# Kernel tuning notes

Measured on AMD Instinct MI355X. Metric: run time of the kernel, lower is better.

The kernel has to match this reference:

```python
import jax, jax.numpy as jnp
import numpy as np

B = 8192
IN = 512          # inputs feature dim (input_size[2])
CTX = 256         # context_input_size
CENTER = 512      # center_size
MIN_ = IN + CTX   # module_input_size = 768
FF = 1024         # n_ff_pre_units
RNN = 1024        # n_rnn_units
OUT = 512         # output_size
O2C = 256         # output_to_center_size
TOT = OUT + O2C   # total_output_size = 768


def setup_inputs() -> dict:
    key = jax.random.key(0)
    ks = jax.random.split(key, 12)
    return {
        "inputs": jax.random.normal(ks[0], (B, 1, IN), jnp.float32),
        "center_state": jax.random.normal(ks[1], (B, 1, CENTER), jnp.float32),
        "module_state": jax.random.normal(ks[2], (B, 1, RNN), jnp.float32),
        # reading_weights: truncated normal stddev 0.1 in TF; plain normal*0.1 is fine for a math reference
        "W_read": jax.random.normal(ks[3], (CENTER, CTX), jnp.float32) * 0.1,
        "W_pre": jax.random.normal(ks[4], (MIN_, FF), jnp.float32) * (1.0 / np.sqrt(MIN_)),
        "b_pre": jnp.zeros((FF,), jnp.float32),
        "Wx": jax.random.normal(ks[5], (FF, RNN), jnp.float32) * (1.0 / np.sqrt(FF)),
        "Wh": jax.random.normal(ks[6], (RNN, RNN), jnp.float32) * (1.0 / np.sqrt(RNN)),
        "b_rnn": jnp.zeros((RNN,), jnp.float32),
        "W_post": jax.random.normal(ks[7], (RNN, TOT), jnp.float32) * (1.0 / np.sqrt(RNN)),
        "b_post": jnp.zeros((TOT,), jnp.float32),
    }


def reference(inputs, center_state, module_state, W_read, W_pre, b_pre, Wx, Wh, b_rnn, W_post, b_post):
    # tf.clip_by_norm(W, 1.0): global Frobenius norm clip
    norm = jnp.sqrt(jnp.sum(W_read * W_read))
    W_clip = W_read * (1.0 / jnp.maximum(norm, 1.0))
    # context read: [B,1,CENTER] @ [CENTER,CTX] -> [B,1,CTX]
    context = jnp.einsum("btc,cd->btd", center_state, W_clip)
    module_inputs = jnp.concatenate([inputs, context], axis=2)  # [B,1,MIN_]
    rnn_in = jax.nn.relu(jnp.einsum("btf,fg->btg", module_inputs, W_pre) + b_pre)
    # SimpleRNNCell: h' = tanh(x Wx + h Wh + b)
    h_new = jnp.tanh(jnp.einsum("btf,fg->btg", rnn_in, Wx)
                     + jnp.einsum("btf,fg->btg", module_state, Wh) + b_rnn)
    module_output = jax.nn.relu(jnp.einsum("btf,fg->btg", h_new, W_post) + b_post)
    network_output = module_output[:, :, :OUT]
    module_output_to_center = module_output[:, :, OUT:]
    return (network_output, module_output_to_center, h_new)
```

## Files before the change

kernel.cpp:

```cpp
#include <hip/hip_runtime.h>

typedef __bf16 bf16x8 __attribute__((ext_vector_type(8)));
typedef float  f32x4  __attribute__((ext_vector_type(4)));
typedef unsigned short ushort8 __attribute__((ext_vector_type(8)));

#define B_ROWS 8192
#define OUT_D  512
#define O2C_D  256
#define TOT_D  768
#define MIN_D  768
#define RNN_D  1024

__device__ __forceinline__ unsigned short f2bf(float f) {
    unsigned int u = __builtin_bit_cast(unsigned int, f);
    u = (u + 0x7fff + ((u >> 16) & 1)) >> 16;
    return (unsigned short)u;
}

__device__ __forceinline__ void load_lds16(const void* g, void* l) {
    __builtin_amdgcn_global_load_lds(
        (const __attribute__((address_space(1))) unsigned int*)g,
        (__attribute__((address_space(3))) unsigned int*)l, 16, 0, 0);
}

__launch_bounds__(256)
__global__ void prep_all(const float* __restrict__ Wread, float* __restrict__ partials,
                         const float* __restrict__ Wpre, const float* __restrict__ Wx,
                         const float* __restrict__ Wh,  const float* __restrict__ Wpost,
                         unsigned short* __restrict__ WpreT, unsigned short* __restrict__ WxhT,
                         unsigned short* __restrict__ WpostT, unsigned short* __restrict__ WreadT,
                         const float* __restrict__ center, const float* __restrict__ inputs,
                         const float* __restrict__ mstate,
                         unsigned short* __restrict__ csB, unsigned short* __restrict__ miB,
                         unsigned short* __restrict__ rnB) {
    const int bid = blockIdx.x;
    const int tid = threadIdx.x;
    if (bid < 128) {
        __shared__ float red[4];
        const float* p = Wread + bid * 1024 + tid * 4;
        f32x4 v = *(const f32x4*)p;
        float s = v[0]*v[0] + v[1]*v[1] + v[2]*v[2] + v[3]*v[3];
        #pragma unroll
        for (int off = 32; off > 0; off >>= 1) s += __shfl_down(s, off, 64);
        if ((tid & 63) == 0) red[tid >> 6] = s;
        __syncthreads();
        if (tid == 0) partials[bid] = red[0] + red[1] + red[2] + red[3];
        return;
    }
    if (bid < 1984) {
        int g = (bid - 128) * 256 + tid;
        const float* W; unsigned short* out; int N, ostride;
        if (g < 98304)        { W = Wpre;  out = WpreT;        N = 1024; ostride = 768;  }
        else if (g < 229376)  { g -= 98304;  W = Wx;    out = WxhT;        N = 1024; ostride = 2048; }
        else if (g < 360448)  { g -= 229376; W = Wh;    out = WxhT + 1024; N = 1024; ostride = 2048; }
        else if (g < 458752)  { g -= 360448; W = Wpost; out = WpostT;      N = 768;  ostride = 1024; }
        else                  { g -= 458752; W = Wread; out = WreadT;      N = 256;  ostride = 512;  }
        int n  = g % N;
        int kg = g / N;
        ushort8 o;
        #pragma unroll
        for (int j = 0; j < 8; ++j)
            o[j] = f2bf(W[(long)(kg * 8 + j) * N + n]);
        *(ushort8*)(out + (long)n * ostride + kg * 8) = o;
        return;
    }
    long g = (long)(bid - 1984) * 256 + tid;
    const float* src; unsigned short* dst; int logc, ostride;
    if (g < 524288)       { src = center; dst = csB;        logc = 9;  ostride = 512;  }
    else if (g < 1048576) { g -= 524288;  src = inputs; dst = miB;        logc = 9;  ostride = 768;  }
    else                  { g -= 1048576; src = mstate; dst = rnB + 1024; logc = 10; ostride = 2048; }
    long e = g * 8;
    long row = e >> logc;
    int  col = (int)(e & ((1 << logc) - 1));
    f32x4 v0 = *(const f32x4*)(src + e);
    f32x4 v1 = *(const f32x4*)(src + e + 4);
    ushort8 o;
    o[0] = f2bf(v0[0]); o[1] = f2bf(v0[1]); o[2] = f2bf(v0[2]); o[3] = f2bf(v0[3]);
    o[4] = f2bf(v1[0]); o[5] = f2bf(v1[1]); o[6] = f2bf(v1[2]); o[7] = f2bf(v1[3]);
    *(ushort8*)(dst + row * (long)ostride + col) = o;
}

template<int MODE, int BNT>
__launch_bounds__(256, 4)
__global__ void gemm_bt(const unsigned short* __restrict__ A,
                        const unsigned short* __restrict__ Bt,
                        int K, const float* __restrict__ bias,
                        unsigned short* __restrict__ outB, int ldob,
                        float* __restrict__ outF, int ldof) {
    constexpr int U   = BNT / 32;
    constexpr int BJ  = BNT / 32;
    __shared__ alignas(16) unsigned short smem[128 * 64 + BNT * 64];
    unsigned short* sA = smem;
    unsigned short* sB = smem + 128 * 64;

    const int tid  = threadIdx.x;
    const int wave = tid >> 6;
    const int lane = tid & 63;
    const int bm = blockIdx.x, bn = blockIdx.y;
    const int wm = wave & 1, wn = wave >> 1;
    const int lr = lane >> 4;
    const int lc = lane & 15;
    const int sw = lc & 7;

    f32x4 acc[4][U] = {};

    long aoff[4], boff[BJ];
    #pragma unroll
    for (int j = 0; j < 4; ++j) {
        const int c   = tid + j * 256;
        const int row = c >> 3;
        const int kg  = (c & 7) ^ (row & 7);
        aoff[j] = (long)(bm * 128 + row) * K + kg * 8;
    }
    #pragma unroll
    for (int j = 0; j < BJ; ++j) {
        const int c   = tid + j * 256;
        const int row = c >> 3;
        const int kg  = (c & 7) ^ (row & 7);
        boff[j] = (long)(bn * BNT + row) * K + kg * 8;
    }

    for (int k0 = 0; k0 < K; k0 += 64) {
        #pragma unroll
        for (int j = 0; j < 4; ++j)
            load_lds16(A + aoff[j] + k0, (char*)sA + j * 4096 + wave * 1024);
        #pragma unroll
        for (int j = 0; j < BJ; ++j)
            load_lds16(Bt + boff[j] + k0, (char*)sB + j * 4096 + wave * 1024);
        __syncthreads();

        #pragma unroll
        for (int kh = 0; kh < 2; ++kh) {
            const int ch = (kh * 4 + lr) ^ sw;
            bf16x8 af[4], bfr[U];
            #pragma unroll
            for (int t = 0; t < 4; ++t)
                af[t] = *(const bf16x8*)(sA + (wm * 64 + t * 16 + lc) * 64 + ch * 8);
            #pragma unroll
            for (int u = 0; u < U; ++u)
                bfr[u] = *(const bf16x8*)(sB + (wn * (BNT / 2) + u * 16 + lc) * 64 + ch * 8);
            #pragma unroll
            for (int i = 0; i < 4; ++i)
                #pragma unroll
                for (int u = 0; u < U; ++u)
                    acc[i][u] = __builtin_amdgcn_mfma_f32_16x16x32_bf16(af[i], bfr[u], acc[i][u], 0, 0, 0);
        }
        __syncthreads();
    }

    float sc = 1.f;
    if constexpr (MODE == 0) {
        float s = 0.f;
        for (int i = 0; i < 128; ++i) s += bias[i];
        sc = 1.f / fmaxf(sqrtf(s), 1.f);
    }
    #pragma unroll
    for (int u = 0; u < U; ++u) {
        float bv = 0.f;
        if constexpr (MODE != 0) bv = bias[bn * BNT + wn * (BNT / 2) + u * 16 + lc];
        #pragma unroll
        for (int tm = 0; tm < 4; ++tm)
            #pragma unroll
            for (int r = 0; r < 4; ++r) {
                float v = acc[tm][u][r];
                if constexpr (MODE == 0) v *= sc;
                else v += bv;
                if constexpr (MODE == 1 || MODE == 3) v = fmaxf(v, 0.f);
                acc[tm][u][r] = v;
            }
    }

    const int ctcol = wn * (BNT / 2);

    if constexpr (MODE <= 2) {
        unsigned short* Cb = smem;
        #pragma unroll
        for (int u = 0; u < U; ++u)
            #pragma unroll
            for (int tm = 0; tm < 4; ++tm)
                #pragma unroll
                for (int r = 0; r < 4; ++r)
                    Cb[(wm * 64 + tm * 16 + lr * 4 + r) * BNT + ctcol + u * 16 + lc] =
                        f2bf(acc[tm][u][r]);
        __syncthreads();
        constexpr int RC = BNT / 8;
        constexpr int CPT = 128 * RC / 256;
        #pragma unroll
        for (int t = 0; t < CPT; ++t) {
            const int chunk = t * 256 + tid;
            const int row = chunk / RC;
            const int c8  = chunk % RC;
            ushort8 val = *(ushort8*)(Cb + row * BNT + c8 * 8);
            *(ushort8*)(outB + (long)(bm * 128 + row) * ldob + bn * BNT + c8 * 8) = val;
        }
    }

    if constexpr (MODE == 3) {
        float* Cf = (float*)smem;
        #pragma unroll
        for (int h = 0; h < 2; ++h) {
            __syncthreads();
            if (wm == h) {
                #pragma unroll
                for (int u = 0; u < U; ++u)
                    #pragma unroll
                    for (int tm = 0; tm < 4; ++tm)
                        #pragma unroll
                        for (int r = 0; r < 4; ++r)
                            Cf[(tm * 16 + lr * 4 + r) * BNT + ctcol + u * 16 + lc] =
                                acc[tm][u][r];
            }
            __syncthreads();
            constexpr int RCF = BNT / 4;
            constexpr int CPTF = 64 * RCF / 256;
            #pragma unroll
            for (int t = 0; t < CPTF; ++t) {
                const int chunk = t * 256 + tid;
                const int row = chunk / RCF;
                const int c4  = chunk % RCF;
                f32x4 val = *(f32x4*)(Cf + row * BNT + c4 * 4);
                const long grow = bm * 128 + h * 64 + row;
                if (bn * BNT < OUT_D)
                    *(f32x4*)(outF + grow * OUT_D + bn * BNT + c4 * 4) = val;
                else
                    *(f32x4*)(outF + (long)B_ROWS * OUT_D + grow * O2C_D
                              + (bn * BNT - OUT_D) + c4 * 4) = val;
            }
        }
    }
}

__launch_bounds__(512, 1)
__global__ void gemm256(const unsigned short* __restrict__ A,
                        const unsigned short* __restrict__ Bt,
                        int K, const float* __restrict__ bias,
                        unsigned short* __restrict__ outB,
                        float* __restrict__ outF) {
    constexpr int ABUF = 256 * 64;
    constexpr int BBUF = 128 * 64;
    constexpr int BUFE = ABUF + BBUF;
    __shared__ alignas(16) unsigned short smem[3 * BUFE];

    const int tid  = threadIdx.x;
    const int wave = tid >> 6;
    const int lane = tid & 63;
    const int bn = blockIdx.x, bm = blockIdx.y;
    const int wm = wave >> 1, wn = wave & 1;
    const int lr = lane >> 4;
    const int lc = lane & 15;
    const int sw = lc & 7;
    const int nt = K >> 6;

    f32x4 acc[4][4] = {};

    long aoff[4], boff[2];
    #pragma unroll
    for (int j = 0; j < 4; ++j) {
        const int c   = tid + j * 512;
        const int row = c >> 3;
        const int kg  = (c & 7) ^ (row & 7);
        aoff[j] = (long)(bm * 256 + row) * K + kg * 8;
    }
    #pragma unroll
    for (int j = 0; j < 2; ++j) {
        const int c   = tid + j * 512;
        const int row = c >> 3;
        const int kg  = (c & 7) ^ (row & 7);
        boff[j] = (long)(bn * 128 + row) * K + kg * 8;
    }

    auto stageA2 = [&](int buf, int k0, int jlo) {
        char* base = (char*)(smem + buf * BUFE);
        load_lds16(A + aoff[jlo]     + k0, base + jlo       * 8192 + wave * 1024);
        load_lds16(A + aoff[jlo + 1] + k0, base + (jlo + 1) * 8192 + wave * 1024);
    };
    auto stageB1 = [&](int buf, int k0, int j) {
        char* base = (char*)(smem + buf * BUFE) + ABUF * 2;
        load_lds16(Bt + boff[j] + k0, base + j * 8192 + wave * 1024);
    };
    auto dsA = [&](int buf, int kh, bf16x8* af) {
        const unsigned short* sA = smem + buf * BUFE;
        const int ch = (kh * 4 + lr) ^ sw;
        #pragma unroll
        for (int m = 0; m < 4; ++m)
            af[m] = *(const bf16x8*)(sA + (wm * 64 + m * 16 + lc) * 64 + ch * 8);
    };
    auto dsB = [&](int buf, int kh, bf16x8* bf) {
        const unsigned short* sB = smem + buf * BUFE + ABUF;
        const int ch = (kh * 4 + lr) ^ sw;
        #pragma unroll
        for (int n = 0; n < 4; ++n)
            bf[n] = *(const bf16x8*)(sB + (wn * 64 + n * 16 + lc) * 64 + ch * 8);
    };

    stageA2(0, 0, 0); stageA2(0, 0, 2); stageB1(0, 0, 0); stageB1(0, 0, 1);
    if (nt > 1) {
        stageA2(1, 64, 0); stageA2(1, 64, 2); stageB1(1, 64, 0); stageB1(1, 64, 1);
        asm volatile("s_waitcnt vmcnt(6)" ::: "memory");
    } else {
        asm volatile("s_waitcnt vmcnt(0)" ::: "memory");
    }
    __builtin_amdgcn_s_barrier();

    int cur = 0;
    for (int t = 0; t < nt; ++t) {
        const int  k2   = (t + 2) << 6;
        const bool st   = (t + 2) < nt;
        const int  nbuf = (cur >= 1) ? cur - 1 : cur + 2;

        bf16x8 af[4], bf[4];

        if (st) { stageA2(nbuf, k2, 0); stageB1(nbuf, k2, 0); }
        dsA(cur, 0, af); dsB(cur, 0, bf);
        __builtin_amdgcn_s_barrier();
        asm volatile("s_waitcnt lgkmcnt(0)" ::: "memory");
        __builtin_amdgcn_sched_barrier(0);
        __builtin_amdgcn_s_setprio(1);
        #pragma unroll
        for (int m = 0; m < 4; ++m)
            #pragma unroll
            for (int n = 0; n < 4; ++n)
                acc[m][n] = __builtin_amdgcn_mfma_f32_16x16x32_bf16(af[m], bf[n], acc[m][n], 0, 0, 0);
        __builtin_amdgcn_s_setprio(0);
        __builtin_amdgcn_s_barrier();

        if (st) { stageA2(nbuf, k2, 2); stageB1(nbuf, k2, 1); }
        dsA(cur, 1, af); dsB(cur, 1, bf);
        if (t + 1 < nt) {
            if (st) asm volatile("s_waitcnt vmcnt(6)" ::: "memory");
            else    asm volatile("s_waitcnt vmcnt(0)" ::: "memory");
        }
        __builtin_amdgcn_s_barrier();
        asm volatile("s_waitcnt lgkmcnt(0)" ::: "memory");
        __builtin_amdgcn_sched_barrier(0);
        __builtin_amdgcn_s_setprio(1);
        #pragma unroll
        for (int m = 0; m < 4; ++m)
            #pragma unroll
            for (int n = 0; n < 4; ++n)
                acc[m][n] = __builtin_amdgcn_mfma_f32_16x16x32_bf16(af[m], bf[n], acc[m][n], 0, 0, 0);
        __builtin_amdgcn_s_setprio(0);
        __builtin_amdgcn_s_barrier();

        cur = (cur == 2) ? 0 : cur + 1;
    }

    #pragma unroll
    for (int n = 0; n < 4; ++n) {
        const float bv = bias[bn * 128 + wn * 64 + n * 16 + lc];
        #pragma unroll
        for (int m = 0; m < 4; ++m)
            #pragma unroll
            for (int r = 0; r < 4; ++r)
                acc[m][n][r] = tanhf(acc[m][n][r] + bv);
    }

    unsigned short* Cb = smem;
    __syncthreads();
    #pragma unroll
    for (int m = 0; m < 4; ++m)
        #pragma unroll
        for (int n = 0; n < 4; ++n)
            #pragma unroll
            for (int r = 0; r < 4; ++r)
                Cb[(wm * 64 + m * 16 + lr * 4 + r) * 128 + wn * 64 + n * 16 + lc] =
                    f2bf(acc[m][n][r]);
    __syncthreads();
    #pragma unroll
    for (int tch = 0; tch < 8; ++tch) {
        const int chunk = tch * 512 + tid;
        const int row = chunk >> 4;
        const int c8  = chunk & 15;
        ushort8 v = *(ushort8*)(Cb + row * 128 + c8 * 8);
        *(ushort8*)(outB + (long)(bm * 256 + row) * RNN_D + bn * 128 + c8 * 8) = v;
    }
    __syncthreads();

    float* Cf = (float*)smem;
    #pragma unroll
    for (int m = 0; m < 4; ++m)
        #pragma unroll
        for (int n = 0; n < 4; ++n)
            #pragma unroll
            for (int r = 0; r < 4; ++r)
                Cf[(wm * 64 + m * 16 + lr * 4 + r) * 128 + wn * 64 + n * 16 + lc] =
                    acc[m][n][r];
    __syncthreads();
    #pragma unroll
    for (int tch = 0; tch < 16; ++tch) {
        const int chunk = tch * 512 + tid;
        const int row = chunk >> 5;
        const int c4  = chunk & 31;
        f32x4 v = *(f32x4*)(Cf + row * 128 + c4 * 4);
        *(f32x4*)(outF + (long)(bm * 256 + row) * RNN_D + bn * 128 + c4 * 4) = v;
    }
}

extern "C" void kernel_launch(void* const* d_in, const int* in_sizes, int n_in,
                              void* d_out, int out_size, void* d_ws, size_t ws_size,
                              hipStream_t stream) {
    const float* inputs = (const float*)d_in[0];
    const float* center = (const float*)d_in[1];
    const float* mstate = (const float*)d_in[2];
    const float* W_read = (const float*)d_in[3];
    const float* W_pre  = (const float*)d_in[4];
    const float* b_pre  = (const float*)d_in[5];
    const float* Wx     = (const float*)d_in[6];
    const float* Wh     = (const float*)d_in[7];
    const float* b_rnn  = (const float*)d_in[8];
    const float* W_post = (const float*)d_in[9];
    const float* b_post = (const float*)d_in[10];
    float* out = (float*)d_out;

    char* ws = (char*)d_ws;
    float* partials = (float*)ws;
    unsigned short* WreadT = (unsigned short*)(ws + 1024);
    unsigned short* WpreT  = WreadT + 256 * 512;
    unsigned short* WxhT   = WpreT  + 1024 * 768;
    unsigned short* WpostT = WxhT   + (long)1024 * 2048;
    unsigned short* csB    = WpostT + 768 * 1024;
    unsigned short* miB    = csB + (long)B_ROWS * 512;
    unsigned short* rnB    = miB + (long)B_ROWS * MIN_D;
    unsigned short* hB     = rnB + (long)B_ROWS * 2048;

    prep_all<<<10176, 256, 0, stream>>>(W_read, partials,
                                        W_pre, Wx, Wh, W_post,
                                        WpreT, WxhT, WpostT, WreadT,
                                        center, inputs, mstate, csB, miB, rnB);

    gemm_bt<0, 64><<<dim3(64, 4), 256, 0, stream>>>(csB, WreadT, 512, partials,
                                                    miB + 512, MIN_D, nullptr, 0);
    gemm_bt<1, 128><<<dim3(64, 8), 256, 0, stream>>>(miB, WpreT, 768, b_pre,
                                                     rnB, 2048, nullptr, 0);
    gemm256<<<dim3(8, 32), 512, 0, stream>>>(rnB, WxhT, 2048, b_rnn,
                                             hB, out + (long)B_ROWS * TOT_D);
    gemm_bt<3, 64><<<dim3(64, 12), 256, 0, stream>>>(hB, WpostT, 1024, b_post,
                                                     nullptr, 0, out, 0);
}
```

Measured before the change: 241.2 us.

## Software-pipeline LDS fragment reads in the recurrent GEMM and remap block order

Restructures the main recurrent GEMM loop so the LDS fragment reads for the next K-half are issued while the MFMAs for the current half run. It uses double register fragments and partial lgkmcnt waits in place of a full wait before each MFMA block. Global-to-LDS staging is merged into a single six-load issue per tile, with one fewer barrier per half. The grid becomes 1D, and block indices are remapped so consecutive blocks share B-column tiles, which should improve L2 reuse. The cost is higher register pressure from holding two fragment sets.

```diff
diff --git a/kernel.cpp b/kernel.cpp
--- a/kernel.cpp
+++ b/kernel.cpp
@@ -244,7 +244,9 @@
     const int tid  = threadIdx.x;
     const int wave = tid >> 6;
     const int lane = tid & 63;
-    const int bn = blockIdx.x, bm = blockIdx.y;
+    const int i  = blockIdx.x;
+    const int bm = (i & 7) + 8 * ((i >> 3) & 3);
+    const int bn = i >> 5;
     const int wm = wave >> 1, wn = wave & 1;
     const int lr = lane >> 4;
     const int lc = lane & 15;
@@ -269,14 +271,15 @@
         boff[j] = (long)(bn * 128 + row) * K + kg * 8;
     }
 
-    auto stageA2 = [&](int buf, int k0, int jlo) {
+    auto stage6 = [&](int buf, int k0) {
         char* base = (char*)(smem + buf * BUFE);
-        load_lds16(A + aoff[jlo]     + k0, base + jlo       * 8192 + wave * 1024);
-        load_lds16(A + aoff[jlo + 1] + k0, base + (jlo + 1) * 8192 + wave * 1024);
-    };
-    auto stageB1 = [&](int buf, int k0, int j) {
-        char* base = (char*)(smem + buf * BUFE) + ABUF * 2;
-        load_lds16(Bt + boff[j] + k0, base + j * 8192 + wave * 1024);
+        #pragma unroll
+        for (int j = 0; j < 4; ++j)
+            load_lds16(A + aoff[j] + k0, base + j * 8192 + wave * 1024);
+        char* bbase = base + ABUF * 2;
+        #pragma unroll
+        for (int j = 0; j < 2; ++j)
+            load_lds16(Bt + boff[j] + k0, bbase + j * 8192 + wave * 1024);
     };
     auto dsA = [&](int buf, int kh, bf16x8* af) {
         const unsigned short* sA = smem + buf * BUFE;
@@ -293,28 +296,9 @@
             bf[n] = *(const bf16x8*)(sB + (wn * 64 + n * 16 + lc) * 64 + ch * 8);
     };
 
-    stageA2(0, 0, 0); stageA2(0, 0, 2); stageB1(0, 0, 0); stageB1(0, 0, 1);
-    if (nt > 1) {
-        stageA2(1, 64, 0); stageA2(1, 64, 2); stageB1(1, 64, 0); stageB1(1, 64, 1);
-        asm volatile("s_waitcnt vmcnt(6)" ::: "memory");
-    } else {
-        asm volatile("s_waitcnt vmcnt(0)" ::: "memory");
-    }
-    __builtin_amdgcn_s_barrier();
-
-    int cur = 0;
-    for (int t = 0; t < nt; ++t) {
-        const int  k2   = (t + 2) << 6;
-        const bool st   = (t + 2) < nt;
-        const int  nbuf = (cur >= 1) ? cur - 1 : cur + 2;
-
-        bf16x8 af[4], bf[4];
-
-        if (st) { stageA2(nbuf, k2, 0); stageB1(nbuf, k2, 0); }
-        dsA(cur, 0, af); dsB(cur, 0, bf);
-        __builtin_amdgcn_s_barrier();
-        asm volatile("s_waitcnt lgkmcnt(0)" ::: "memory");
-        __builtin_amdgcn_sched_barrier(0);
+    bf16x8 af0[4], bf0[4], af1[4], bf1[4];
+
+    auto mfma16 = [&](const bf16x8* af, const bf16x8* bf) {
         __builtin_amdgcn_s_setprio(1);
         #pragma unroll
         for (int m = 0; m < 4; ++m)
@@ -322,27 +306,42 @@
             for (int n = 0; n < 4; ++n)
                 acc[m][n] = __builtin_amdgcn_mfma_f32_16x16x32_bf16(af[m], bf[n], acc[m][n], 0, 0, 0);
         __builtin_amdgcn_s_setprio(0);
-        __builtin_amdgcn_s_barrier();
-
-        if (st) { stageA2(nbuf, k2, 2); stageB1(nbuf, k2, 1); }
-        dsA(cur, 1, af); dsB(cur, 1, bf);
+    };
+
+    stage6(0, 0);
+    stage6(1, 64);
+    asm volatile("s_waitcnt vmcnt(6)" ::: "memory");
+    __builtin_amdgcn_s_barrier();
+    dsA(0, 0, af0); dsB(0, 0, bf0);
+
+    int cur = 0, nxt = 1;
+    for (int t = 0; t < nt; ++t) {
+        const bool st = (t + 2) < nt;
+        const int  nbuf = (cur >= 1) ? cur - 1 : 2;
+
+        if (st) stage6(nbuf, (t + 2) << 6);
+        dsA(cur, 1, af1); dsB(cur, 1, bf1);
+        asm volatile("s_waitcnt lgkmcnt(8)" ::: "memory");
+        __builtin_amdgcn_sched_barrier(0);
+        mfma16(af0, bf0);
         if (t + 1 < nt) {
             if (st) asm volatile("s_waitcnt vmcnt(6)" ::: "memory");
             else    asm volatile("s_waitcnt vmcnt(0)" ::: "memory");
         }
         __builtin_amdgcn_s_barrier();
-        asm volatile("s_waitcnt lgkmcnt(0)" ::: "memory");
+
+        if (t + 1 < nt) {
+            dsA(nxt, 0, af0); dsB(nxt, 0, bf0);
+            asm volatile("s_waitcnt lgkmcnt(8)" ::: "memory");
+        } else {
+            asm volatile("s_waitcnt lgkmcnt(0)" ::: "memory");
+        }
         __builtin_amdgcn_sched_barrier(0);
-        __builtin_amdgcn_s_setprio(1);
-        #pragma unroll
-        for (int m = 0; m < 4; ++m)
-            #pragma unroll
-            for (int n = 0; n < 4; ++n)
-                acc[m][n] = __builtin_amdgcn_mfma_f32_16x16x32_bf16(af[m], bf[n], acc[m][n], 0, 0, 0);
-        __builtin_amdgcn_s_setprio(0);
+        mfma16(af1, bf1);
         __builtin_amdgcn_s_barrier();
 
-        cur = (cur == 2) ? 0 : cur + 1;
+        cur = nxt;
+        nxt = (nxt == 2) ? 0 : nxt + 1;
     }
 
     #pragma unroll
@@ -432,8 +431,8 @@
                                                     miB + 512, MIN_D, nullptr, 0);
     gemm_bt<1, 128><<<dim3(64, 8), 256, 0, stream>>>(miB, WpreT, 768, b_pre,
                                                      rnB, 2048, nullptr, 0);
-    gemm256<<<dim3(8, 32), 512, 0, stream>>>(rnB, WxhT, 2048, b_rnn,
-                                             hB, out + (long)B_ROWS * TOT_D);
+    gemm256<<<256, 512, 0, stream>>>(rnB, WxhT, 2048, b_rnn,
+                                     hB, out + (long)B_ROWS * TOT_D);
     gemm_bt<3, 64><<<dim3(64, 12), 256, 0, stream>>>(hB, WpostT, 1024, b_post,
                                                      nullptr, 0, out, 0);
 }
```

New measurement: 241.7 us. About the same (+0.2%).
